# Optimization experiments

Hardware: AMD Instinct MI355X
Metric: run time of the kernel (lower is better)

Reference implementation:

```python
import jax, jax.numpy as jnp
import numpy as np

DIM = 128      # embedding dim (c)
HEAD_DIM = 32
NH = DIM // HEAD_DIM          # 4 mLSTM heads
INNER = 256                    # round_up(2*DIM, 64)
DH = INNER // NH               # 64 per-head dim
K = 4                          # causal conv kernel size
BS = 4                         # qkv_proj_blocksize
NB = INNER // BS               # 64 block-diagonal qkv blocks
B, T, H, W = 8, 16, 32, 32


def setup_inputs() -> dict:
    key = jax.random.key(0)
    ks = jax.random.split(key, 12)
    s = 0.02
    return {
        "x": jax.random.normal(ks[0], (B, DIM, T, H, W), jnp.float32),
        "W_up": jax.random.normal(ks[1], (DIM, 2 * INNER), jnp.float32) * s,
        "conv_w": jax.random.normal(ks[2], (K, 1, INNER), jnp.float32) * s,  # depthwise causal conv (WIO)
        "conv_b": jnp.zeros((INNER,), jnp.float32),
        "Wq": jax.random.normal(ks[3], (NB, BS, BS), jnp.float32) * s,  # block-diag headwise linear
        "Wk": jax.random.normal(ks[4], (NB, BS, BS), jnp.float32) * s,
        "Wv": jax.random.normal(ks[5], (NB, BS, BS), jnp.float32) * s,
        "ig_w": jax.random.normal(ks[6], (3 * INNER, NH), jnp.float32) * s,
        "ig_b": jnp.zeros((NH,), jnp.float32),
        "fg_w": jax.random.normal(ks[7], (3 * INNER, NH), jnp.float32) * s,
        "fg_b": jnp.zeros((NH,), jnp.float32),
        "ln_w": jnp.ones((INNER,), jnp.float32),   # multi-head layernorm scale
        "skip": jnp.ones((INNER,), jnp.float32),   # learnable skip
        "W_down": jax.random.normal(ks[8], (INNER, DIM), jnp.float32) * s,
    }


def _headwise(y, Wh):
    # block-diagonal linear: y [B,S,INNER] split into NB blocks of BS
    Bx, S, _ = y.shape
    yb = y.reshape(Bx, S, NB, BS)
    return jnp.einsum('bsni,noi->bsno', yb, Wh).reshape(Bx, S, INNER)


def _mlstm_parallel(q, k, v, ig, fg):
    # q,k,v: [B,NH,S,DH]; ig,fg (gate preacts): [B,NH,S]
    S = q.shape[2]
    log_f = jax.nn.log_sigmoid(fg)
    lf_cum = jnp.concatenate(
        [jnp.zeros_like(log_f[..., :1]), jnp.cumsum(log_f, axis=-1)], axis=-1)  # [B,NH,S+1]
    logfg = lf_cum[..., 1:, None] - lf_cum[..., None, 1:]                      # [B,NH,S,S]
    mask = jnp.tril(jnp.ones((S, S), bool))
    logfg = jnp.where(mask, logfg, -jnp.inf)
    log_D = logfg + ig[..., None, :]
    max_log_D = jnp.max(log_D, axis=-1, keepdims=True)
    Dmat = jnp.exp(log_D - max_log_D)
    qk = jnp.einsum('bhsd,bhtd->bhst', q, k) / jnp.sqrt(jnp.float32(q.shape[-1]))
    C = qk * Dmat
    normalizer = jnp.maximum(jnp.abs(C.sum(-1, keepdims=True)), jnp.exp(-max_log_D))
    return jnp.einsum('bhst,bhtd->bhsd', C / (normalizer + 1e-6), v)


def _forward(x, W_up, conv_w, conv_b, Wq, Wk, Wv, ig_w, ig_b, fg_w, fg_b, ln_w, skip, W_down):
    b, c, t, hh, ww = x.shape
    xs = jnp.transpose(x, (0, 3, 4, 2, 1)).reshape(b * hh * ww, t, c)  # (b h w) t c
    up = xs @ W_up
    x_m, z = jnp.split(up, 2, axis=-1)                                  # [Bx,S,INNER] each
    # depthwise causal conv + swish
    xc = jax.lax.conv_general_dilated(
        x_m, conv_w, (1,), [(K - 1, 0)],
        dimension_numbers=('NWC', 'WIO', 'NWC'), feature_group_count=INNER) + conv_b
    xc = jax.nn.silu(xc)
    q = _headwise(xc, Wq)
    k = _headwise(xc, Wk)
    v = _headwise(x_m, Wv)
    if_in = jnp.concatenate([q, k, v], axis=-1)
    ig = if_in @ ig_w + ig_b                                            # [Bx,S,NH]
    fg = if_in @ fg_w + fg_b
    Bx, S = q.shape[0], q.shape[1]
    qh = q.reshape(Bx, S, NH, DH).transpose(0, 2, 1, 3)
    kh = k.reshape(Bx, S, NH, DH).transpose(0, 2, 1, 3)
    vh = v.reshape(Bx, S, NH, DH).transpose(0, 2, 1, 3)
    ht = _mlstm_parallel(qh, kh, vh, ig.transpose(0, 2, 1), fg.transpose(0, 2, 1))  # [Bx,NH,S,DH]
    # multi-head (group) layernorm over DH, weight only
    mu = ht.mean(-1, keepdims=True)
    var = ht.var(-1, keepdims=True)
    hn = (ht - mu) / jnp.sqrt(var + 1e-5) * ln_w.reshape(NH, DH)[None, :, None, :]
    hn = hn.transpose(0, 2, 1, 3).reshape(Bx, S, INNER)
    h_state = (hn + skip * xc) * jax.nn.silu(z)
    out = h_state @ W_down                                              # [Bx,S,DIM]
    return out.reshape(b, hh, ww, t, c).transpose(0, 4, 3, 1, 2)        # b c t h w


def reference(x, W_up, conv_w, conv_b, Wq, Wk, Wv, ig_w, ig_b, fg_w, fg_b, ln_w, skip, W_down):
    return _forward(x, W_up, conv_w, conv_b, Wq, Wk, Wv, ig_w, ig_b, fg_w, fg_b, ln_w, skip, W_down)
```

## Files before the change

### kernel.cpp

```cpp
#include <hip/hip_runtime.h>
#include <hip/hip_bf16.h>
#include <cmath>


typedef __attribute__((ext_vector_type(8))) short short8;
typedef __attribute__((ext_vector_type(4))) short short4v;
typedef __attribute__((ext_vector_type(4))) float f32x4;
typedef unsigned short ushort_t;

static __device__ __forceinline__ float siluf(float v) {
  return v / (1.0f + __expf(-v));
}
static __device__ __forceinline__ float logsigf(float v) {
  return fminf(v, 0.f) - log1pf(__expf(-fabsf(v)));
}
static __device__ __forceinline__ float sel4(float4 w, int idx) {
  float r = w.x;
  r = (idx == 1) ? w.y : r;
  r = (idx == 2) ? w.z : r;
  r = (idx == 3) ? w.w : r;
  return r;
}
static __device__ __forceinline__ ushort_t f2bf(float x) {
  unsigned u = __float_as_uint(x);
  return (ushort_t)((u + 0x7fffu + ((u >> 16) & 1u)) >> 16);
}
static __device__ __forceinline__ float bf2f(ushort_t h) {
  return __uint_as_float(((unsigned)h) << 16);
}
static __device__ __forceinline__ ushort2 pk2bf(float a, float b) {
  union { __hip_bfloat162 v; ushort2 u; } cv;
  cv.v = __float22bfloat162_rn(make_float2(a, b));
  return cv.u;
}
#define DPPF(x, ctrl) \
  __int_as_float(__builtin_amdgcn_mov_dpp(__float_as_int(x), (ctrl), 0xF, 0xF, true))

__global__ __launch_bounds__(256)
void prep_w(const float* __restrict__ Wup, const float* __restrict__ Wd,
            const float* __restrict__ igw, const float* __restrict__ fgw,
            ushort_t* __restrict__ wt_hi, ushort_t* __restrict__ wt_lo,
            ushort_t* __restrict__ wdt_hi, ushort_t* __restrict__ wdt_lo,
            ushort_t* __restrict__ wgf)
{
  const int g = blockIdx.x * 256 + threadIdx.x;
  if (g < 65536) {
    const int jj = g >> 7, c = g & 127;
    const float w = Wup[c*512 + jj];
    const ushort_t h = f2bf(w);
    wt_hi[g] = h;
    wt_lo[g] = f2bf(w - bf2f(h));
  } else if (g < 98304) {
    const int g2 = g - 65536;
    const int c = g2 >> 8, jj = g2 & 255;
    const float w = Wd[jj*128 + c];
    const ushort_t h = f2bf(w);
    wdt_hi[g2] = h;
    wdt_lo[g2] = f2bf(w - bf2f(h));
  } else if (g < 110592) {
    const int e = g - 98304;
    const int kc = e >> 9;
    const int lane = (e >> 3) & 63;
    const int i = e & 7;
    const int n = lane & 15;
    const int kq = kc*32 + (lane >> 4)*8 + i;
    float val = 0.f;
    if (n < 4)      val = igw[kq*4 + n];
    else if (n < 8) val = fgw[kq*4 + (n - 4)];
    wgf[e] = f2bf(val);
  }
}

#define AS 72

__global__ __launch_bounds__(256, 3)
void up_gemm(const float* __restrict__ x,
             const ushort_t* __restrict__ wt_hi, const ushort_t* __restrict__ wt_lo,
             ushort_t* __restrict__ xmb, ushort_t* __restrict__ szb)
{
  __shared__ ushort_t sAhi[128*AS];
  __shared__ ushort_t sAlo[128*AS];

  const int tid = threadIdx.x;
  const int hw0 = blockIdx.x * 128;
  const int j0  = blockIdx.y * 128;
  const int bt  = blockIdx.z;
  const int b   = bt >> 4, t = bt & 15;

  const int wv = tid >> 6;
  const int wm = wv >> 1, wn = wv & 1;
  const int ln = tid & 63;
  const int lm = ln & 15;
  const int q  = ln >> 4;

  const int hwL = tid & 127;
  const int cg  = tid >> 7;

  f32x4 acc[4][4];
  #pragma unroll
  for (int i = 0; i < 4; ++i)
    #pragma unroll
    for (int k = 0; k < 4; ++k) acc[i][k] = (f32x4){0.f, 0.f, 0.f, 0.f};

  for (int stage = 0; stage < 2; ++stage) {
    float xv[8][4];
    {
      const float* xb = &x[((b*128 + stage*64)*16 + t)*1024 + hw0 + hwL];
      #pragma unroll
      for (int p = 0; p < 8; ++p) {
        const float* xp = xb + (p*8 + cg*4)*16384;
        xv[p][0] = xp[0];
        xv[p][1] = xp[16384];
        xv[p][2] = xp[32768];
        xv[p][3] = xp[49152];
      }
    }
    #pragma unroll
    for (int p = 0; p < 8; ++p) {
      const int cl = p*8 + cg*4;
      const float v0 = xv[p][0], v1 = xv[p][1], v2 = xv[p][2], v3 = xv[p][3];
      const ushort2 h01 = pk2bf(v0, v1);
      const ushort2 h23 = pk2bf(v2, v3);
      const ushort2 l01 = pk2bf(v0 - bf2f(h01.x), v1 - bf2f(h01.y));
      const ushort2 l23 = pk2bf(v2 - bf2f(h23.x), v3 - bf2f(h23.y));
      *(ushort4*)&sAhi[hwL*AS + cl] = make_ushort4(h01.x, h01.y, h23.x, h23.y);
      *(ushort4*)&sAlo[hwL*AS + cl] = make_ushort4(l01.x, l01.y, l23.x, l23.y);
    }
    __syncthreads();

    #pragma unroll
    for (int s = 0; s < 2; ++s) {
      const int kc = s*32 + q*8;
      const int kg = stage*64 + kc;
      short8 bh[4], bl[4];
      #pragma unroll
      for (int nt = 0; nt < 4; ++nt) {
        const int jr = j0 + wn*64 + nt*16 + lm;
        bh[nt] = *(const short8*)&wt_hi[jr*128 + kg];
        bl[nt] = *(const short8*)&wt_lo[jr*128 + kg];
      }
      #pragma unroll
      for (int mt = 0; mt < 4; ++mt) {
        const int ao = (wm*64 + mt*16 + lm)*AS + kc;
        const short8 ah = *(const short8*)&sAhi[ao];
        const short8 al = *(const short8*)&sAlo[ao];
        #pragma unroll
        for (int nt = 0; nt < 4; ++nt) {
          acc[mt][nt] = __builtin_amdgcn_mfma_f32_16x16x32_bf16(ah, bh[nt], acc[mt][nt], 0, 0, 0);
          acc[mt][nt] = __builtin_amdgcn_mfma_f32_16x16x32_bf16(ah, bl[nt], acc[mt][nt], 0, 0, 0);
          acc[mt][nt] = __builtin_amdgcn_mfma_f32_16x16x32_bf16(al, bh[nt], acc[mt][nt], 0, 0, 0);
        }
      }
    }
    __syncthreads();
  }

  const bool isz = (j0 >= 256);
  #pragma unroll
  for (int mt = 0; mt < 4; ++mt) {
    #pragma unroll
    for (int nt = 0; nt < 4; ++nt) {
      const int jc = j0 + wn*64 + nt*16 + lm;
      #pragma unroll
      for (int r = 0; r < 4; ++r) {
        const int rowg = bt*1024 + hw0 + wm*64 + mt*16 + q*4 + r;
        const float v = acc[mt][nt][r];
        if (!isz) xmb[rowg*256 + jc] = f2bf(v);
        else      szb[rowg*256 + (jc - 256)] = f2bf(siluf(v));
      }
    }
  }
}

#define SQ 264
#define SXC 260

__global__ __launch_bounds__(256, 4)
void seq_kernel(const ushort_t* __restrict__ xm_ws,
                ushort_t* szh,
                const float* __restrict__ conv_w, const float* __restrict__ conv_b,
                const float* __restrict__ Wq, const float* __restrict__ Wk,
                const float* __restrict__ Wv,
                const ushort_t* __restrict__ wgf,
                const float* __restrict__ igb, const float* __restrict__ fgb,
                const float* __restrict__ lnw, const float* __restrict__ skipw)
{
  __shared__ __align__(16) ushort_t q_lds[16*SQ];
  __shared__ __align__(16) ushort_t k_lds[16*SQ];
  __shared__ __align__(16) ushort_t v_lds[16*SQ];
  __shared__ __align__(16) ushort_t xc_lds[16*SXC];
  __shared__ __align__(16) ushort_t p_lds[4*16*36];
  __shared__ __align__(16) float s_gpart[512];
  __shared__ float s_ig[64];
  __shared__ float s_lf[64];

  const int tid = threadIdx.x;
  const int j   = tid;
  const int l2  = j & 3;
  const int seq = blockIdx.x;
  const int rbase = (seq >> 10) * 16384 + (seq & 1023);

  const int w    = tid >> 6;
  const int ln   = tid & 63;
  const int g    = ln >> 4;
  const int lc   = ln & 15;
  const int hb2  = w * 64;

  const float4 wq4 = *(const float4*)&Wq[j*4];
  const float4 wk4 = *(const float4*)&Wk[j*4];
  const float4 wv4 = *(const float4*)&Wv[j*4];
  float wqp[4], wkp[4], wvp[4];
  #pragma unroll
  for (int d = 0; d < 4; ++d) {
    const int idx = l2 ^ d;
    wqp[d] = sel4(wq4, idx);
    wkp[d] = sel4(wk4, idx);
    wvp[d] = sel4(wv4, idx);
  }
  const float cw0 = conv_w[j],     cw1 = conv_w[256+j];
  const float cw2 = conv_w[512+j], cw3 = conv_w[768+j];
  const float cb  = conv_b[j];

  ushort_t mh[8];
  #pragma unroll
  for (int t = 0; t < 8; ++t)
    mh[t] = xm_ws[(rbase + t*1024)*256 + j];

  float p1 = 0.f, p2 = 0.f, p3 = 0.f;
  #pragma unroll
  for (int t = 0; t < 16; ++t) {
    const float m = bf2f(mh[t & 7]);
    if (t < 8) mh[t & 7] = xm_ws[(rbase + (t+8)*1024)*256 + j];
    const float pre = cw0*p3 + cw1*p2 + cw2*p1 + cw3*m + cb;
    const float x = siluf(pre);
    p3 = p2; p2 = p1; p1 = m;
    const float x1 = DPPF(x, 0xB1), x2 = DPPF(x, 0x4E), x3 = DPPF(x, 0x1B);
    const float m1 = DPPF(m, 0xB1), m2 = DPPF(m, 0x4E), m3 = DPPF(m, 0x1B);
    const float qv = x*wqp[0] + x1*wqp[1] + x2*wqp[2] + x3*wqp[3];
    const float kv = x*wkp[0] + x1*wkp[1] + x2*wkp[2] + x3*wkp[3];
    const float vv = m*wvp[0] + m1*wvp[1] + m2*wvp[2] + m3*wvp[3];
    q_lds [t*SQ  + j] = f2bf(qv);
    k_lds [t*SQ  + j] = f2bf(kv);
    v_lds [t*SQ  + j] = f2bf(vv);
    xc_lds[t*SXC + j] = f2bf(x);
  }
  __syncthreads();

  f32x4 gacc = (f32x4){0.f, 0.f, 0.f, 0.f};
  #pragma unroll
  for (int c6 = 0; c6 < 6; ++c6) {
    const int kc = w*6 + c6;
    const ushort_t* yb = (kc < 8) ? q_lds : (kc < 16) ? k_lds : v_lds;
    const int klocal = (kc & 7)*32;
    const short8 ya = *(const short8*)&yb[lc*SQ + klocal + g*8];
    const short8 wb = *(const short8*)&wgf[(kc*64 + ln)*8];
    gacc = __builtin_amdgcn_mfma_f32_16x16x32_bf16(ya, wb, gacc, 0, 0, 0);
  }
  f32x4 qkacc = (f32x4){0.f, 0.f, 0.f, 0.f};
  {
    const short8 qa0 = *(const short8*)&q_lds[lc*SQ + hb2 + g*8];
    const short8 qa1 = *(const short8*)&q_lds[lc*SQ + hb2 + 32 + g*8];
    const short8 kb0 = *(const short8*)&k_lds[lc*SQ + hb2 + g*8];
    const short8 kb1 = *(const short8*)&k_lds[lc*SQ + hb2 + 32 + g*8];
    qkacc = __builtin_amdgcn_mfma_f32_16x16x32_bf16(qa0, kb0, qkacc, 0, 0, 0);
    qkacc = __builtin_amdgcn_mfma_f32_16x16x32_bf16(qa1, kb1, qkacc, 0, 0, 0);
  }
  if (lc < 8) {
    #pragma unroll
    for (int r = 0; r < 4; ++r)
      s_gpart[w*128 + (g*4 + r)*8 + lc] = gacc[r];
  }
  __syncthreads();

  if (tid < 128) {
    const int t = tid >> 3, n = tid & 7;
    const float s = s_gpart[t*8+n] + s_gpart[128 + t*8+n]
                  + s_gpart[256 + t*8+n] + s_gpart[384 + t*8+n];
    if (n < 4) s_ig[t*4 + n] = s + igb[n];
    else       s_lf[t*4 + (n-4)] = logsigf(s + fgb[n-4]);
  }
  __syncthreads();

  float* s_lfc = s_gpart;
  if (tid < 4) {
    float run = 0.f;
    s_lfc[tid] = 0.f;
    #pragma unroll
    for (int t = 0; t < 16; ++t) { run += s_lf[t*4 + tid]; s_lfc[(t+1)*4 + tid] = run; }
  }
  __syncthreads();

  {
    const int tcol = lc;
    const float lfc_t1 = s_lfc[(tcol+1)*4 + w];
    const float igt    = s_ig[tcol*4 + w];
    float ld[4], mloc[4];
    #pragma unroll
    for (int r = 0; r < 4; ++r) {
      const int s = g*4 + r;
      const float lfs = s_lfc[(s+1)*4 + w];
      ld[r] = (tcol <= s) ? (lfs - lfc_t1 + igt) : -INFINITY;
      mloc[r] = ld[r];
    }
    #pragma unroll
    for (int r = 0; r < 4; ++r) {
      mloc[r] = fmaxf(mloc[r], DPPF(mloc[r], 0xB1));
      mloc[r] = fmaxf(mloc[r], DPPF(mloc[r], 0x4E));
      mloc[r] = fmaxf(mloc[r], __shfl_xor(mloc[r], 4));
      mloc[r] = fmaxf(mloc[r], DPPF(mloc[r], 0x128));
    }
    float cs[4], rsum[4];
    #pragma unroll
    for (int r = 0; r < 4; ++r) {
      const int s = g*4 + r;
      cs[r] = (tcol <= s) ? (qkacc[r] * 0.125f) * __expf(ld[r] - mloc[r]) : 0.f;
      rsum[r] = cs[r];
    }
    #pragma unroll
    for (int r = 0; r < 4; ++r) {
      rsum[r] += DPPF(rsum[r], 0xB1);
      rsum[r] += DPPF(rsum[r], 0x4E);
      rsum[r] += __shfl_xor(rsum[r], 4);
      rsum[r] += DPPF(rsum[r], 0x128);
    }
    #pragma unroll
    for (int r = 0; r < 4; ++r) {
      const float denom = fmaxf(fabsf(rsum[r]), __expf(-mloc[r])) + 1e-6f;
      const float pv = cs[r] / denom;
      p_lds[(w*16 + g*4 + r)*36 + tcol] = f2bf(pv);
    }
  }
  __syncthreads();

  f32x4 oacc[4];
  #pragma unroll
  for (int c = 0; c < 4; ++c) oacc[c] = (f32x4){0.f, 0.f, 0.f, 0.f};
  {
    const int tb = g*8;
    short8 pa = (short8){0,0,0,0,0,0,0,0};
    if (tb < 16) {
      const short4v plo = *(const short4v*)&p_lds[(w*16 + lc)*36 + tb];
      const short4v phi = *(const short4v*)&p_lds[(w*16 + lc)*36 + tb + 4];
      pa[0]=plo[0]; pa[1]=plo[1]; pa[2]=plo[2]; pa[3]=plo[3];
      pa[4]=phi[0]; pa[5]=phi[1]; pa[6]=phi[2]; pa[7]=phi[3];
    }
    #pragma unroll
    for (int c = 0; c < 4; ++c) {
      short8 vb;
      #pragma unroll
      for (int i = 0; i < 8; ++i)
        vb[i] = (short)v_lds[((tb + i) & 15)*SQ + hb2 + c*16 + lc];
      oacc[c] = __builtin_amdgcn_mfma_f32_16x16x32_bf16(pa, vb, oacc[c], 0, 0, 0);
    }
  }

  float lnc[4], skc[4];
  #pragma unroll
  for (int c = 0; c < 4; ++c) {
    const int ch = hb2 + c*16 + lc;
    lnc[c] = lnw[ch];
    skc[c] = skipw[ch];
  }
  #pragma unroll
  for (int r = 0; r < 4; ++r) {
    const int s = g*4 + r;
    float tot = oacc[0][r] + oacc[1][r] + oacc[2][r] + oacc[3][r];
    tot += DPPF(tot, 0xB1);
    tot += DPPF(tot, 0x4E);
    tot += __shfl_xor(tot, 4);
    tot += DPPF(tot, 0x128);
    const float mu = tot * (1.f/64.f);
    float var = 0.f;
    #pragma unroll
    for (int c = 0; c < 4; ++c) { const float d = oacc[c][r] - mu; var += d*d; }
    var += DPPF(var, 0xB1);
    var += DPPF(var, 0x4E);
    var += __shfl_xor(var, 4);
    var += DPPF(var, 0x128);
    const float rstd = rsqrtf(var * (1.f/64.f) + 1e-5f);
    #pragma unroll
    for (int c = 0; c < 4; ++c) {
      const int ch = hb2 + c*16 + lc;
      const float hn = (oacc[c][r] - mu) * rstd * lnc[c];
      const float xcv = bf2f(xc_lds[s*SXC + ch]);
      q_lds[s*SQ + ch] = f2bf(hn + skc[c]*xcv);
    }
  }
  __syncthreads();

  #pragma unroll
  for (int s = 0; s < 16; ++s) {
    const long long og = (long long)(rbase + s*1024)*256 + tid;
    const float szv = bf2f(szh[og]);
    const float hv  = bf2f(q_lds[s*SQ + tid]);
    szh[og] = f2bf(hv * szv);
  }
}

__global__ __launch_bounds__(256, 3)
void down_gemm(const ushort_t* __restrict__ hb,
               const ushort_t* __restrict__ wdt_hi, const ushort_t* __restrict__ wdt_lo,
               float* __restrict__ out)
{
  const int tid = threadIdx.x;
  const int hw0 = blockIdx.x * 128;
  const int bt  = blockIdx.z;
  const int bq  = bt >> 4, tq = bt & 15;
  const int rowbase = bt*1024 + hw0;

  const int wv = tid >> 6;
  const int wm = wv >> 1, wn = wv & 1;
  const int ln = tid & 63;
  const int lm = ln & 15;
  const int q  = ln >> 4;

  f32x4 acc[4][4];
  #pragma unroll
  for (int i = 0; i < 4; ++i)
    #pragma unroll
    for (int k = 0; k < 4; ++k) acc[i][k] = (f32x4){0.f, 0.f, 0.f, 0.f};

  #pragma unroll 2
  for (int kc = 0; kc < 256; kc += 32) {
    const int kq = kc + q*8;
    short8 ah[4], al[4];
    #pragma unroll
    for (int mt = 0; mt < 4; ++mt) {
      const int c = wm*64 + mt*16 + lm;
      ah[mt] = *(const short8*)&wdt_hi[c*256 + kq];
      al[mt] = *(const short8*)&wdt_lo[c*256 + kq];
    }
    #pragma unroll
    for (int nt = 0; nt < 4; ++nt) {
      const int n = wn*64 + nt*16 + lm;
      const short8 bf = *(const short8*)&hb[(rowbase + n)*256 + kq];
      #pragma unroll
      for (int mt = 0; mt < 4; ++mt) {
        acc[mt][nt] = __builtin_amdgcn_mfma_f32_16x16x32_bf16(ah[mt], bf, acc[mt][nt], 0, 0, 0);
        acc[mt][nt] = __builtin_amdgcn_mfma_f32_16x16x32_bf16(al[mt], bf, acc[mt][nt], 0, 0, 0);
      }
    }
  }

  #pragma unroll
  for (int mt = 0; mt < 4; ++mt) {
    #pragma unroll
    for (int nt = 0; nt < 4; ++nt) {
      const int hw = hw0 + wn*64 + nt*16 + lm;
      #pragma unroll
      for (int r = 0; r < 4; ++r) {
        const int c = wm*64 + mt*16 + q*4 + r;
        out[((bq*128 + c)*16 + tq)*1024 + hw] = acc[mt][nt][r];
      }
    }
  }
}

extern "C" void kernel_launch(void* const* d_in, const int* in_sizes, int n_in,
                              void* d_out, int out_size, void* d_ws, size_t ws_size,
                              hipStream_t stream)
{
  const float* x      = (const float*)d_in[0];
  const float* Wup    = (const float*)d_in[1];
  const float* conv_w = (const float*)d_in[2];
  const float* conv_b = (const float*)d_in[3];
  const float* Wq     = (const float*)d_in[4];
  const float* Wk     = (const float*)d_in[5];
  const float* Wv     = (const float*)d_in[6];
  const float* igw    = (const float*)d_in[7];
  const float* igb    = (const float*)d_in[8];
  const float* fgw    = (const float*)d_in[9];
  const float* fgb    = (const float*)d_in[10];
  const float* lnw    = (const float*)d_in[11];
  const float* skipw  = (const float*)d_in[12];
  const float* Wd     = (const float*)d_in[13];
  float* out = (float*)d_out;

  ushort_t* xmb    = (ushort_t*)d_ws;
  ushort_t* szb    = xmb + 33554432;
  ushort_t* wt_hi  = (ushort_t*)((char*)d_ws + 134217728);
  ushort_t* wt_lo  = wt_hi + 65536;
  ushort_t* wdt_hi = wt_lo + 65536;
  ushort_t* wdt_lo = wdt_hi + 32768;
  ushort_t* wgf    = wdt_lo + 32768;

  prep_w<<<432, 256, 0, stream>>>(Wup, Wd, igw, fgw,
                                  wt_hi, wt_lo, wdt_hi, wdt_lo, wgf);
  up_gemm<<<dim3(8, 4, 128), 256, 0, stream>>>(x, wt_hi, wt_lo, xmb, szb);
  seq_kernel<<<8192, 256, 0, stream>>>(xmb, szb,
                                       conv_w, conv_b, Wq, Wk, Wv,
                                       wgf, igb, fgb, lnw, skipw);
  down_gemm<<<dim3(8, 1, 128), 256, 0, stream>>>(szb, wdt_hi, wdt_lo, out);
}
```

Measured before the change: 369.6 us.

## Fuse gate reduction with DPP prefix scan and pack bf16 conversions in seq kernel

Merges the gate-partial reduction and the serial forget-gate cumulative sum into one step, using a DPP row-shift inclusive scan across 16 lanes, which removes one barrier and a single-thread serial loop. Removes a barrier between the P-matrix write and the PV MFMA stage on the basis that each wave reads only its own rows. Replaces scalar float-to-bf16 conversions with a packed two-value conversion helper throughout. Dropping the barrier depends on wave-local LDS visibility, and the DPP scan depends on correct row_shr semantics.

New measurement: 365.2 us. About the same (-1.2%).

```diff
diff --git a/kernel.cpp b/kernel.cpp
--- a/kernel.cpp
+++ b/kernel.cpp
@@ -192,7 +192,6 @@
   __shared__ __align__(16) ushort_t p_lds[4*16*36];
   __shared__ __align__(16) float s_gpart[512];
   __shared__ float s_ig[64];
-  __shared__ float s_lf[64];
 
   const int tid = threadIdx.x;
   const int j   = tid;
@@ -239,10 +238,12 @@
     const float qv = x*wqp[0] + x1*wqp[1] + x2*wqp[2] + x3*wqp[3];
     const float kv = x*wkp[0] + x1*wkp[1] + x2*wkp[2] + x3*wkp[3];
     const float vv = m*wvp[0] + m1*wvp[1] + m2*wvp[2] + m3*wvp[3];
-    q_lds [t*SQ  + j] = f2bf(qv);
-    k_lds [t*SQ  + j] = f2bf(kv);
-    v_lds [t*SQ  + j] = f2bf(vv);
-    xc_lds[t*SXC + j] = f2bf(x);
+    const ushort2 qk = pk2bf(qv, kv);
+    const ushort2 vx = pk2bf(vv, x);
+    q_lds [t*SQ  + j] = qk.x;
+    k_lds [t*SQ  + j] = qk.y;
+    v_lds [t*SQ  + j] = vx.x;
+    xc_lds[t*SXC + j] = vx.y;
   }
   __syncthreads();
 
@@ -272,21 +273,21 @@
   }
   __syncthreads();
 
-  if (tid < 128) {
-    const int t = tid >> 3, n = tid & 7;
-    const float s = s_gpart[t*8+n] + s_gpart[128 + t*8+n]
-                  + s_gpart[256 + t*8+n] + s_gpart[384 + t*8+n];
-    if (n < 4) s_ig[t*4 + n] = s + igb[n];
-    else       s_lf[t*4 + (n-4)] = logsigf(s + fgb[n-4]);
-  }
-  __syncthreads();
-
   float* s_lfc = s_gpart;
-  if (tid < 4) {
-    float run = 0.f;
-    s_lfc[tid] = 0.f;
-    #pragma unroll
-    for (int t = 0; t < 16; ++t) { run += s_lf[t*4 + tid]; s_lfc[(t+1)*4 + tid] = run; }
+  if (tid < 64) {
+    const int t = tid & 15, h = tid >> 4;
+    const float si = s_gpart[t*8 + h]       + s_gpart[128 + t*8 + h]
+                   + s_gpart[256 + t*8 + h] + s_gpart[384 + t*8 + h];
+    const float sf = s_gpart[t*8 + 4 + h]       + s_gpart[128 + t*8 + 4 + h]
+                   + s_gpart[256 + t*8 + 4 + h] + s_gpart[384 + t*8 + 4 + h];
+    s_ig[t*4 + h] = si + igb[h];
+    float lf = logsigf(sf + fgb[h]);
+    lf += DPPF(lf, 0x111);
+    lf += DPPF(lf, 0x112);
+    lf += DPPF(lf, 0x114);
+    lf += DPPF(lf, 0x118);
+    s_lfc[(t+1)*4 + h] = lf;
+    if (t == 0) s_lfc[h] = 0.f;
   }
   __syncthreads();
 
@@ -323,14 +324,19 @@
       rsum[r] += __shfl_xor(rsum[r], 4);
       rsum[r] += DPPF(rsum[r], 0x128);
     }
+    float pvv[4];
     #pragma unroll
     for (int r = 0; r < 4; ++r) {
       const float denom = fmaxf(fabsf(rsum[r]), __expf(-mloc[r])) + 1e-6f;
-      const float pv = cs[r] / denom;
-      p_lds[(w*16 + g*4 + r)*36 + tcol] = f2bf(pv);
-    }
-  }
-  __syncthreads();
+      pvv[r] = cs[r] / denom;
+    }
+    const ushort2 p01 = pk2bf(pvv[0], pvv[1]);
+    const ushort2 p23 = pk2bf(pvv[2], pvv[3]);
+    p_lds[(w*16 + g*4 + 0)*36 + tcol] = p01.x;
+    p_lds[(w*16 + g*4 + 1)*36 + tcol] = p01.y;
+    p_lds[(w*16 + g*4 + 2)*36 + tcol] = p23.x;
+    p_lds[(w*16 + g*4 + 3)*36 + tcol] = p23.y;
+  }
 
   f32x4 oacc[4];
   #pragma unroll
@@ -378,22 +384,34 @@
     var += __shfl_xor(var, 4);
     var += DPPF(var, 0x128);
     const float rstd = rsqrtf(var * (1.f/64.f) + 1e-5f);
+    float hval[4];
     #pragma unroll
     for (int c = 0; c < 4; ++c) {
       const int ch = hb2 + c*16 + lc;
       const float hn = (oacc[c][r] - mu) * rstd * lnc[c];
       const float xcv = bf2f(xc_lds[s*SXC + ch]);
-      q_lds[s*SQ + ch] = f2bf(hn + skc[c]*xcv);
-    }
+      hval[c] = hn + skc[c]*xcv;
+    }
+    const ushort2 h01 = pk2bf(hval[0], hval[1]);
+    const ushort2 h23 = pk2bf(hval[2], hval[3]);
+    q_lds[s*SQ + hb2 + 0*16 + lc] = h01.x;
+    q_lds[s*SQ + hb2 + 1*16 + lc] = h01.y;
+    q_lds[s*SQ + hb2 + 2*16 + lc] = h23.x;
+    q_lds[s*SQ + hb2 + 3*16 + lc] = h23.y;
   }
   __syncthreads();
 
   #pragma unroll
-  for (int s = 0; s < 16; ++s) {
-    const long long og = (long long)(rbase + s*1024)*256 + tid;
-    const float szv = bf2f(szh[og]);
-    const float hv  = bf2f(q_lds[s*SQ + tid]);
-    szh[og] = f2bf(hv * szv);
+  for (int s = 0; s < 16; s += 2) {
+    const long long og0 = (long long)(rbase + s*1024)*256 + tid;
+    const long long og1 = (long long)(rbase + (s+1)*1024)*256 + tid;
+    const float szv0 = bf2f(szh[og0]);
+    const float szv1 = bf2f(szh[og1]);
+    const float hv0  = bf2f(q_lds[s*SQ + tid]);
+    const float hv1  = bf2f(q_lds[(s+1)*SQ + tid]);
+    const ushort2 hs = pk2bf(hv0 * szv0, hv1 * szv1);
+    szh[og0] = hs.x;
+    szh[og1] = hs.y;
   }
 }
 
```
